# Optimization experiments

Hardware: AMD Instinct MI355X
Metric: run time of the kernel (lower is better)

Reference implementation:

```python
import jax, jax.numpy as jnp
import numpy as np

N = 100000
F_IN = 128
HIDDEN = 64
HEADS = 4
EPS = 1e-16
SLOPE = 0.2  # PyG GATConv default negative_slope


def gat_conv(x, src, dst, W, a_src, a_dst, b, heads, out_ch, concat, n_nodes):
    # x: [N, F]; W: [F, heads*out_ch]; a_src/a_dst: [heads, out_ch]
    h = (x @ W).reshape(n_nodes, heads, out_ch)              # [N, H, C]
    alpha_s = jnp.einsum('nhc,hc->nh', h, a_src)             # [N, H]
    alpha_d = jnp.einsum('nhc,hc->nh', h, a_dst)             # [N, H]
    e = alpha_s[src] + alpha_d[dst]                          # [E, H]
    e = jnp.where(e > 0, e, SLOPE * e)                       # leaky_relu
    # segment softmax over destination node
    m = jax.ops.segment_max(e, dst, num_segments=n_nodes)    # [N, H]
    m = jnp.where(jnp.isfinite(m), m, 0.0)                   # empty segments
    ex = jnp.exp(e - m[dst])                                 # [E, H]
    denom = jax.ops.segment_sum(ex, dst, num_segments=n_nodes)  # [N, H]
    alpha = ex / (denom[dst] + EPS)                          # [E, H]
    # weighted scatter-aggregate of source features at destinations
    msg = h[src] * alpha[:, :, None]                         # [E, H, C]
    out = jax.ops.segment_sum(msg, dst, num_segments=n_nodes)  # [N, H, C]
    if concat:
        out = out.reshape(n_nodes, heads * out_ch)
    else:
        out = out.mean(axis=1)
    return out + b


def setup_inputs() -> dict:
    key = jax.random.key(0)
    ks = jax.random.split(key, 12)
    x = jax.random.normal(ks[0], (N, F_IN), dtype=jnp.float32)
    edge_index = jax.random.randint(ks[1], (2, 1600000), 0, N, dtype=jnp.int64)
    s1 = 1.0 / np.sqrt(F_IN)
    s2 = 1.0 / np.sqrt(HIDDEN)
    return {
        'x': x,
        'edge_index': edge_index,
        'W1': jax.random.normal(ks[2], (F_IN, HIDDEN), dtype=jnp.float32) * s1,
        'a_src1': jax.random.normal(ks[3], (HEADS, HIDDEN // HEADS), dtype=jnp.float32) * s2,
        'a_dst1': jax.random.normal(ks[4], (HEADS, HIDDEN // HEADS), dtype=jnp.float32) * s2,
        'b1': jnp.zeros((HIDDEN,), dtype=jnp.float32),
        'W2': jax.random.normal(ks[5], (HIDDEN, HIDDEN), dtype=jnp.float32) * s2,
        'a_src2': jax.random.normal(ks[6], (1, HIDDEN), dtype=jnp.float32) * s2,
        'a_dst2': jax.random.normal(ks[7], (1, HIDDEN), dtype=jnp.float32) * s2,
        'b2': jnp.zeros((HIDDEN,), dtype=jnp.float32),
        'Wc': jax.random.normal(ks[8], (HIDDEN, 1), dtype=jnp.float32) * s2,
        'bc': jnp.zeros((1,), dtype=jnp.float32),
    }


def reference(x, edge_index, W1, a_src1, a_dst1, b1, W2, a_src2, a_dst2, b2, Wc, bc):
    src, dst = edge_index[0], edge_index[1]
    # dropout layers are identity in eval mode
    h = gat_conv(x, src, dst, W1, a_src1, a_dst1, b1,
                 heads=HEADS, out_ch=HIDDEN // HEADS, concat=True, n_nodes=N)
    h = jax.nn.relu(h)
    h = gat_conv(h, src, dst, W2, a_src2, a_dst2, b2,
                 heads=1, out_ch=HIDDEN, concat=False, n_nodes=N)
    h = jax.nn.relu(h)
    return h @ Wc + bc  # [N, 1]
```

## Files before the change

kernel.cpp:

```cpp
#include <hip/hip_runtime.h>
#include <hip/hip_bf16.h>


typedef __hip_bfloat16 bf16;
typedef unsigned short ushort;
typedef unsigned char uchar;
typedef __attribute__((ext_vector_type(8))) short short8;
typedef __attribute__((ext_vector_type(4))) float f32x4;

#define NN 100000
#define EE 1600000
#define BKB 9
#define BKN (1 << BKB)
#define NBK ((NN + BKN - 1) >> BKB)
#define CAP 10240
#define TILE 4096
#define EPT 16
#define NT ((EE + TILE - 1) / TILE)
#define BN 16
#define CHE 512

__device__ __forceinline__ float relu_np(float v) { return (v < 0.f) ? 0.f : v; }
__device__ __forceinline__ float lrelu(float v) { return v > 0.f ? v : 0.2f * v; }
__device__ __forceinline__ ushort f2bf(float f) {
    __hip_bfloat16 h = __float2bfloat16(f);
    return *reinterpret_cast<ushort*>(&h);
}
__device__ __forceinline__ float bf2f(ushort u) {
    unsigned int x = ((unsigned int)u) << 16;
    return __uint_as_float(x);
}

__global__ __launch_bounds__(256) void k_init(
    int* __restrict__ gcur, const float* __restrict__ W2,
    const float* __restrict__ aS2, const float* __restrict__ aD2,
    ushort* __restrict__ wExt)
{
    const int tid = threadIdx.x;
    if (tid < NBK) gcur[tid] = tid * CAP;
    for (int i = tid; i < 80 * 64; i += 256) {
        int n = i >> 6, k = i & 63;
        float v = 0.f;
        if (n < 64) {
            v = W2[k * 64 + n];
        } else if (n == 64) {
            for (int c = 0; c < 64; ++c) v = fmaf(W2[k * 64 + c], aS2[c], v);
        } else if (n == 65) {
            for (int c = 0; c < 64; ++c) v = fmaf(W2[k * 64 + c], aD2[c], v);
        }
        wExt[i] = f2bf(v);
    }
}

__global__ __launch_bounds__(256) void k_part(
    const int* __restrict__ src, const int* __restrict__ dst,
    int* __restrict__ gcur, int* __restrict__ pairs, int E)
{
    __shared__ int lh[NBK];
    __shared__ int lbase[NBK];
    const int tid = threadIdx.x;
    for (int i = tid; i < NBK; i += 256) lh[i] = 0;
    __syncthreads();
    const int e0 = blockIdx.x * TILE;
    int pk[EPT], bk[EPT], rv[EPT];
    #pragma unroll
    for (int j = 0; j < EPT; ++j) {
        int e = e0 + j * 256 + tid;
        if (e < E) {
            int d = dst[e];
            bk[j] = d >> BKB;
            pk[j] = src[e] | ((d & (BKN - 1)) << 17);
            rv[j] = atomicAdd(&lh[bk[j]], 1);
        }
    }
    __syncthreads();
    for (int i = tid; i < NBK; i += 256)
        lbase[i] = lh[i] ? atomicAdd(&gcur[i], lh[i]) : 0;
    __syncthreads();
    #pragma unroll
    for (int j = 0; j < EPT; ++j) {
        int e = e0 + j * 256 + tid;
        if (e < E) pairs[lbase[bk[j]] + rv[j]] = pk[j];
    }
}

__global__ __launch_bounds__(256) void k_bucket(
    const int* __restrict__ gcur, const int* __restrict__ pairs,
    int* __restrict__ row_ptr, uchar* __restrict__ rcnt,
    int* __restrict__ col, int N)
{
    __shared__ int hist[BKN];
    __shared__ int sP[256];
    const int b = blockIdx.x;
    const int n0 = b << BKB;
    const int tid = threadIdx.x;
    const int base = b * CAP, endE = gcur[b];
    for (int i = tid; i < BKN; i += 256) hist[i] = 0;
    __syncthreads();
    for (int i = base + tid; i < endE; i += 256)
        atomicAdd(&hist[pairs[i] >> 17], 1);
    __syncthreads();
    int a0 = hist[2 * tid], a1 = hist[2 * tid + 1];
    int tot = a0 + a1;
    sP[tid] = tot;
    __syncthreads();
    for (int off = 1; off < 256; off <<= 1) {
        int t = (tid >= off) ? sP[tid - off] : 0;
        __syncthreads();
        sP[tid] += t;
        __syncthreads();
    }
    const int excl = sP[tid] - tot;
    const int c0 = base + excl;
    hist[2 * tid] = c0;
    hist[2 * tid + 1] = c0 + a0;
    if (n0 + 2 * tid < N) {
        row_ptr[n0 + 2 * tid] = c0;
        rcnt[n0 + 2 * tid] = (uchar)a0;
    }
    if (n0 + 2 * tid + 1 < N) {
        row_ptr[n0 + 2 * tid + 1] = c0 + a0;
        rcnt[n0 + 2 * tid + 1] = (uchar)a1;
    }
    __syncthreads();
    for (int i = base + tid; i < endE; i += 256) {
        int pr = pairs[i];
        int p = atomicAdd(&hist[pr >> 17], 1);
        col[p] = pr & 0x1FFFF;
    }
}

__global__ __launch_bounds__(256) void k_gemm1(
    const float* __restrict__ x, const float* __restrict__ W1,
    const float* __restrict__ aS, const float* __restrict__ aD,
    ushort* __restrict__ h1, float* __restrict__ as1, float* __restrict__ ad1,
    int N)
{
    __shared__ ushort wB[64 * 128];
    __shared__ ushort wE[16 * 128];
    const int tid = threadIdx.x;
    for (int i = tid; i < 128 * 64; i += 256) {
        int k = i >> 6, n = i & 63;
        wB[n * 128 + k] = f2bf(W1[i]);
    }
    for (int i = tid; i < 128 * 16; i += 256) {
        int k = i >> 4, j = i & 15;
        float v = 0.f;
        if (j < 8) {
            int h = j & 3;
            const float* av = (j < 4) ? aS : aD;
            for (int c = 0; c < 16; ++c)
                v = fmaf(W1[k * 64 + h * 16 + c], av[h * 16 + c], v);
        }
        wE[j * 128 + k] = f2bf(v);
    }
    __syncthreads();
    const int w = tid >> 6, lane = tid & 63;
    const int m = lane & 15, quad = lane >> 4;
    const int ntiles = N >> 4;
    for (int tile = blockIdx.x * 4 + w; tile < ntiles; tile += gridDim.x * 4) {
        const int row0 = tile << 4;
        f32x4 acc[4] = {f32x4{0,0,0,0}, f32x4{0,0,0,0},
                        f32x4{0,0,0,0}, f32x4{0,0,0,0}};
        f32x4 acc5 = {0, 0, 0, 0};
        const float* xp = x + (size_t)(row0 + m) * 128 + quad * 8;
        #pragma unroll
        for (int ks = 0; ks < 128; ks += 32) {
            f32x4 x0 = *(const f32x4*)(xp + ks);
            f32x4 x1 = *(const f32x4*)(xp + ks + 4);
            short8 a;
            #pragma unroll
            for (int j = 0; j < 4; ++j) a[j] = (short)f2bf(x0[j]);
            #pragma unroll
            for (int j = 0; j < 4; ++j) a[4 + j] = (short)f2bf(x1[j]);
            #pragma unroll
            for (int t = 0; t < 4; ++t) {
                short8 b = *(const short8*)&wB[(t * 16 + m) * 128 + ks + quad * 8];
                acc[t] = __builtin_amdgcn_mfma_f32_16x16x32_bf16(a, b, acc[t], 0, 0, 0);
            }
            short8 b5 = *(const short8*)&wE[m * 128 + ks + quad * 8];
            acc5 = __builtin_amdgcn_mfma_f32_16x16x32_bf16(a, b5, acc5, 0, 0, 0);
        }
        #pragma unroll
        for (int t = 0; t < 4; ++t)
            #pragma unroll
            for (int r = 0; r < 4; ++r)
                h1[(size_t)(row0 + quad * 4 + r) * 64 + t * 16 + m] = f2bf(acc[t][r]);
        #pragma unroll
        for (int r = 0; r < 4; ++r) {
            int row = row0 + quad * 4 + r;
            if (m < 4) as1[row * 4 + m] = acc5[r];
            else if (m < 8) ad1[row * 4 + (m - 4)] = acc5[r];
        }
    }
}

__global__ __launch_bounds__(256, 8) void k_seg1f(
    const int* __restrict__ rp, const uchar* __restrict__ rcnt,
    const int* __restrict__ col,
    const float* __restrict__ as1, const float* __restrict__ ad1,
    const ushort* __restrict__ h1, const float* __restrict__ b1,
    const ushort* __restrict__ wExt,
    ushort* __restrict__ h2, float* __restrict__ as2, float* __restrict__ ad2,
    int N)
{
    __shared__ __align__(16) ushort zS[BN * 72];
    __shared__ float pS[CHE * 4];
    __shared__ int colS[CHE];
    __shared__ uchar ndS[CHE];
    __shared__ int sRp[BN + 1];
    __shared__ float bS[64];
    __shared__ float adS[BN * 4];

    const int tid = threadIdx.x;
    const int n0 = blockIdx.x * BN;

    if (tid < 64) bS[tid] = b1[tid];
    if (tid < BN * 4) adS[tid] = ad1[(size_t)n0 * 4 + tid];
    if (tid < BN) sRp[tid] = rp[n0 + tid];
    if (tid == BN) sRp[BN] = rp[n0 + BN - 1] + (int)rcnt[n0 + BN - 1];
    __syncthreads();

    const int eb0 = sRp[0];
    const int cnt = min(sRp[BN] - eb0, CHE);

    for (int t = tid; t < cnt; t += 256) {
        int ge = eb0 + t;
        colS[t] = col[ge];
        int nd = 0;
        #pragma unroll
        for (int k = 1; k < BN; ++k) nd += (ge >= sRp[k]);
        ndS[t] = (uchar)nd;
    }
    __syncthreads();
    for (int t = tid; t < cnt * 4; t += 256) {
        int e = t >> 2, hh = t & 3;
        float v = as1[(size_t)colS[e] * 4 + hh] + adS[ndS[e] * 4 + hh];
        pS[t] = __expf(lrelu(v));
    }
    __syncthreads();

    const int w = tid >> 6, lane = tid & 63;
    const int g = lane >> 4, c4 = lane & 15, head = c4 >> 2;
    const int nb = w * 4 + g;
    const int s_n = sRp[nb] - eb0, e_n = sRp[nb + 1] - eb0;

    f32x4 acc = {0, 0, 0, 0};
    float den = 0.f;
    int i = s_n;
    for (; i + 3 < e_n; i += 4) {
        int cA = colS[i], cB = colS[i + 1], cC = colS[i + 2], cD = colS[i + 3];
        ushort4 hA = *(const ushort4*)&h1[(size_t)cA * 64 + c4 * 4];
        ushort4 hB = *(const ushort4*)&h1[(size_t)cB * 64 + c4 * 4];
        ushort4 hC = *(const ushort4*)&h1[(size_t)cC * 64 + c4 * 4];
        ushort4 hD = *(const ushort4*)&h1[(size_t)cD * 64 + c4 * 4];
        float pA = pS[(i + 0) * 4 + head], pB = pS[(i + 1) * 4 + head];
        float pC = pS[(i + 2) * 4 + head], pD = pS[(i + 3) * 4 + head];
        den += (pA + pB) + (pC + pD);
        acc[0] = fmaf(pA, bf2f(hA.x), acc[0]);
        acc[1] = fmaf(pA, bf2f(hA.y), acc[1]);
        acc[2] = fmaf(pA, bf2f(hA.z), acc[2]);
        acc[3] = fmaf(pA, bf2f(hA.w), acc[3]);
        acc[0] = fmaf(pB, bf2f(hB.x), acc[0]);
        acc[1] = fmaf(pB, bf2f(hB.y), acc[1]);
        acc[2] = fmaf(pB, bf2f(hB.z), acc[2]);
        acc[3] = fmaf(pB, bf2f(hB.w), acc[3]);
        acc[0] = fmaf(pC, bf2f(hC.x), acc[0]);
        acc[1] = fmaf(pC, bf2f(hC.y), acc[1]);
        acc[2] = fmaf(pC, bf2f(hC.z), acc[2]);
        acc[3] = fmaf(pC, bf2f(hC.w), acc[3]);
        acc[0] = fmaf(pD, bf2f(hD.x), acc[0]);
        acc[1] = fmaf(pD, bf2f(hD.y), acc[1]);
        acc[2] = fmaf(pD, bf2f(hD.z), acc[2]);
        acc[3] = fmaf(pD, bf2f(hD.w), acc[3]);
    }
    for (; i < e_n; ++i) {
        int cA = colS[i];
        ushort4 hA = *(const ushort4*)&h1[(size_t)cA * 64 + c4 * 4];
        float pA = pS[i * 4 + head];
        den += pA;
        acc[0] = fmaf(pA, bf2f(hA.x), acc[0]);
        acc[1] = fmaf(pA, bf2f(hA.y), acc[1]);
        acc[2] = fmaf(pA, bf2f(hA.z), acc[2]);
        acc[3] = fmaf(pA, bf2f(hA.w), acc[3]);
    }
    {
        float inv = 1.f / (den + 1e-16f);
        ushort4 zv;
        zv.x = f2bf(relu_np(acc[0] * inv + bS[c4 * 4 + 0]));
        zv.y = f2bf(relu_np(acc[1] * inv + bS[c4 * 4 + 1]));
        zv.z = f2bf(relu_np(acc[2] * inv + bS[c4 * 4 + 2]));
        zv.w = f2bf(relu_np(acc[3] * inv + bS[c4 * 4 + 3]));
        *(ushort4*)&zS[nb * 72 + c4 * 4] = zv;
    }
    __syncthreads();

    const int m = c4, quad = g;
    for (int t = w; t < 5; t += 4) {
        f32x4 acct = {0, 0, 0, 0};
        #pragma unroll
        for (int ks = 0; ks < 64; ks += 32) {
            short8 a = *(const short8*)&zS[m * 72 + ks + quad * 8];
            short8 b = *(const short8*)&wExt[(t * 16 + m) * 64 + ks + quad * 8];
            acct = __builtin_amdgcn_mfma_f32_16x16x32_bf16(a, b, acct, 0, 0, 0);
        }
        if (t < 4) {
            #pragma unroll
            for (int r = 0; r < 4; ++r)
                h2[(size_t)(n0 + quad * 4 + r) * 64 + t * 16 + m] = f2bf(acct[r]);
        } else {
            #pragma unroll
            for (int r = 0; r < 4; ++r) {
                int row = n0 + quad * 4 + r;
                if (m == 0) as2[row] = acct[r];
                else if (m == 1) ad2[row] = acct[r];
            }
        }
    }
}

__global__ __launch_bounds__(256, 8) void k_seg2f(
    const int* __restrict__ rp, const uchar* __restrict__ rcnt,
    const int* __restrict__ col,
    const float* __restrict__ as2, const float* __restrict__ ad2,
    const ushort* __restrict__ h2, const float* __restrict__ b2,
    const float* __restrict__ Wc, const float* __restrict__ bc,
    float* __restrict__ out, int N)
{
    __shared__ float pS[CHE];
    __shared__ int colS[CHE];
    __shared__ uchar ndS[CHE];
    __shared__ int sRp[BN + 1];
    __shared__ float adS[BN];
    __shared__ float b2S[64];
    __shared__ float wcS[64];

    const int tid = threadIdx.x;
    const int n0 = blockIdx.x * BN;
    if (tid < 64) { b2S[tid] = b2[tid]; wcS[tid] = Wc[tid]; }
    if (tid < BN) { sRp[tid] = rp[n0 + tid]; adS[tid] = ad2[n0 + tid]; }
    if (tid == BN) sRp[BN] = rp[n0 + BN - 1] + (int)rcnt[n0 + BN - 1];
    __syncthreads();

    const int eb0 = sRp[0];
    const int cnt = min(sRp[BN] - eb0, CHE);
    for (int t = tid; t < cnt; t += 256) {
        int ge = eb0 + t;
        colS[t] = col[ge];
        int nd = 0;
        #pragma unroll
        for (int k = 1; k < BN; ++k) nd += (ge >= sRp[k]);
        ndS[t] = (uchar)nd;
    }
    __syncthreads();
    for (int t = tid; t < cnt; t += 256)
        pS[t] = __expf(lrelu(as2[colS[t]] + adS[ndS[t]]));
    __syncthreads();

    const int w = tid >> 6, lane = tid & 63;
    const int g = lane >> 4, c4 = lane & 15;
    const int nb = w * 4 + g;
    const int myn = n0 + nb;
    const int s_n = sRp[nb] - eb0, e_n = sRp[nb + 1] - eb0;

    f32x4 acc = {0, 0, 0, 0};
    float den = 0.f;
    int i = s_n;
    for (; i + 3 < e_n; i += 4) {
        int cA = colS[i], cB = colS[i + 1], cC = colS[i + 2], cD = colS[i + 3];
        ushort4 hA = *(const ushort4*)&h2[(size_t)cA * 64 + c4 * 4];
        ushort4 hB = *(const ushort4*)&h2[(size_t)cB * 64 + c4 * 4];
        ushort4 hC = *(const ushort4*)&h2[(size_t)cC * 64 + c4 * 4];
        ushort4 hD = *(const ushort4*)&h2[(size_t)cD * 64 + c4 * 4];
        float pA = pS[i + 0], pB = pS[i + 1], pC = pS[i + 2], pD = pS[i + 3];
        den += (pA + pB) + (pC + pD);
        acc[0] = fmaf(pA, bf2f(hA.x), acc[0]);
        acc[1] = fmaf(pA, bf2f(hA.y), acc[1]);
        acc[2] = fmaf(pA, bf2f(hA.z), acc[2]);
        acc[3] = fmaf(pA, bf2f(hA.w), acc[3]);
        acc[0] = fmaf(pB, bf2f(hB.x), acc[0]);
        acc[1] = fmaf(pB, bf2f(hB.y), acc[1]);
        acc[2] = fmaf(pB, bf2f(hB.z), acc[2]);
        acc[3] = fmaf(pB, bf2f(hB.w), acc[3]);
        acc[0] = fmaf(pC, bf2f(hC.x), acc[0]);
        acc[1] = fmaf(pC, bf2f(hC.y), acc[1]);
        acc[2] = fmaf(pC, bf2f(hC.z), acc[2]);
        acc[3] = fmaf(pC, bf2f(hC.w), acc[3]);
        acc[0] = fmaf(pD, bf2f(hD.x), acc[0]);
        acc[1] = fmaf(pD, bf2f(hD.y), acc[1]);
        acc[2] = fmaf(pD, bf2f(hD.z), acc[2]);
        acc[3] = fmaf(pD, bf2f(hD.w), acc[3]);
    }
    for (; i < e_n; ++i) {
        int cA = colS[i];
        ushort4 hA = *(const ushort4*)&h2[(size_t)cA * 64 + c4 * 4];
        float pA = pS[i];
        den += pA;
        acc[0] = fmaf(pA, bf2f(hA.x), acc[0]);
        acc[1] = fmaf(pA, bf2f(hA.y), acc[1]);
        acc[2] = fmaf(pA, bf2f(hA.z), acc[2]);
        acc[3] = fmaf(pA, bf2f(hA.w), acc[3]);
    }

    float inv = 1.f / (den + 1e-16f);
    float t2 = 0.f;
    #pragma unroll
    for (int j = 0; j < 4; ++j)
        t2 += relu_np(acc[j] * inv + b2S[c4 * 4 + j]) * wcS[c4 * 4 + j];
    t2 += __shfl_xor(t2, 1);
    t2 += __shfl_xor(t2, 2);
    t2 += __shfl_xor(t2, 4);
    t2 += __shfl_xor(t2, 8);
    if (c4 == 0) out[myn] = t2 + bc[0];
}

extern "C" void kernel_launch(void* const* d_in, const int* in_sizes, int n_in,
                              void* d_out, int out_size, void* d_ws, size_t ws_size,
                              hipStream_t stream)
{
    const float* x   = (const float*)d_in[0];
    const int*   ei  = (const int*)d_in[1];
    const float* W1  = (const float*)d_in[2];
    const float* aS1 = (const float*)d_in[3];
    const float* aD1 = (const float*)d_in[4];
    const float* b1  = (const float*)d_in[5];
    const float* W2  = (const float*)d_in[6];
    const float* aS2 = (const float*)d_in[7];
    const float* aD2 = (const float*)d_in[8];
    const float* b2  = (const float*)d_in[9];
    const float* Wc  = (const float*)d_in[10];
    const float* bc  = (const float*)d_in[11];
    float* out = (float*)d_out;

    const int N = NN;
    const int E = EE;
    const int* src = ei;
    const int* dst = ei + E;

    ushort* h1   = (ushort*)d_ws;
    ushort* h2   = h1 + (size_t)N * 64;
    float*  as1  = (float*)(h2 + (size_t)N * 64);
    float*  ad1  = as1 + (size_t)N * 4;
    float*  as2  = ad1 + (size_t)N * 4;
    float*  ad2  = as2 + (size_t)N;
    ushort* wExt = (ushort*)(ad2 + (size_t)N);
    int* row_ptr = (int*)(wExt + 80 * 64);
    uchar* rcnt  = (uchar*)(row_ptr + N);
    int* gcur    = (int*)(rcnt + ((N + 3) & ~3));
    int* col     = gcur + NBK;
    int* pairs   = (int*)h2;

    k_init<<<1, 256, 0, stream>>>(gcur, W2, aS2, aD2, wExt);
    k_part<<<NT, 256, 0, stream>>>(src, dst, gcur, pairs, E);
    k_bucket<<<NBK, 256, 0, stream>>>(gcur, pairs, row_ptr, rcnt, col, N);

    k_gemm1<<<782, 256, 0, stream>>>(x, W1, aS1, aD1, h1, as1, ad1, N);

    k_seg1f<<<N / BN, 256, 0, stream>>>(row_ptr, rcnt, col, as1, ad1, h1, b1,
                                        wExt, h2, as2, ad2, N);

    k_seg2f<<<N / BN, 256, 0, stream>>>(row_ptr, rcnt, col, as2, ad2, h2,
                                        b2, Wc, bc, out, N);
}
```

Measured before the change: 267.8 us.

## Fuse graph partitioning and bucketing with GEMM1 halves into shared launches

```diff
diff --git a/kernel.cpp b/kernel.cpp
--- a/kernel.cpp
+++ b/kernel.cpp
@@ -17,6 +17,8 @@
 #define TILE 4096
 #define EPT 16
 #define NT ((EE + TILE - 1) / TILE)
+#define GH 391
+#define GT 782
 #define BN 16
 #define CHE 512
 
@@ -31,113 +33,12 @@
     return __uint_as_float(x);
 }
 
-__global__ __launch_bounds__(256) void k_init(
-    int* __restrict__ gcur, const float* __restrict__ W2,
-    const float* __restrict__ aS2, const float* __restrict__ aD2,
-    ushort* __restrict__ wExt)
-{
-    const int tid = threadIdx.x;
-    if (tid < NBK) gcur[tid] = tid * CAP;
-    for (int i = tid; i < 80 * 64; i += 256) {
-        int n = i >> 6, k = i & 63;
-        float v = 0.f;
-        if (n < 64) {
-            v = W2[k * 64 + n];
-        } else if (n == 64) {
-            for (int c = 0; c < 64; ++c) v = fmaf(W2[k * 64 + c], aS2[c], v);
-        } else if (n == 65) {
-            for (int c = 0; c < 64; ++c) v = fmaf(W2[k * 64 + c], aD2[c], v);
-        }
-        wExt[i] = f2bf(v);
-    }
-}
-
-__global__ __launch_bounds__(256) void k_part(
-    const int* __restrict__ src, const int* __restrict__ dst,
-    int* __restrict__ gcur, int* __restrict__ pairs, int E)
-{
-    __shared__ int lh[NBK];
-    __shared__ int lbase[NBK];
-    const int tid = threadIdx.x;
-    for (int i = tid; i < NBK; i += 256) lh[i] = 0;
-    __syncthreads();
-    const int e0 = blockIdx.x * TILE;
-    int pk[EPT], bk[EPT], rv[EPT];
-    #pragma unroll
-    for (int j = 0; j < EPT; ++j) {
-        int e = e0 + j * 256 + tid;
-        if (e < E) {
-            int d = dst[e];
-            bk[j] = d >> BKB;
-            pk[j] = src[e] | ((d & (BKN - 1)) << 17);
-            rv[j] = atomicAdd(&lh[bk[j]], 1);
-        }
-    }
-    __syncthreads();
-    for (int i = tid; i < NBK; i += 256)
-        lbase[i] = lh[i] ? atomicAdd(&gcur[i], lh[i]) : 0;
-    __syncthreads();
-    #pragma unroll
-    for (int j = 0; j < EPT; ++j) {
-        int e = e0 + j * 256 + tid;
-        if (e < E) pairs[lbase[bk[j]] + rv[j]] = pk[j];
-    }
-}
-
-__global__ __launch_bounds__(256) void k_bucket(
-    const int* __restrict__ gcur, const int* __restrict__ pairs,
-    int* __restrict__ row_ptr, uchar* __restrict__ rcnt,
-    int* __restrict__ col, int N)
-{
-    __shared__ int hist[BKN];
-    __shared__ int sP[256];
-    const int b = blockIdx.x;
-    const int n0 = b << BKB;
-    const int tid = threadIdx.x;
-    const int base = b * CAP, endE = gcur[b];
-    for (int i = tid; i < BKN; i += 256) hist[i] = 0;
-    __syncthreads();
-    for (int i = base + tid; i < endE; i += 256)
-        atomicAdd(&hist[pairs[i] >> 17], 1);
-    __syncthreads();
-    int a0 = hist[2 * tid], a1 = hist[2 * tid + 1];
-    int tot = a0 + a1;
-    sP[tid] = tot;
-    __syncthreads();
-    for (int off = 1; off < 256; off <<= 1) {
-        int t = (tid >= off) ? sP[tid - off] : 0;
-        __syncthreads();
-        sP[tid] += t;
-        __syncthreads();
-    }
-    const int excl = sP[tid] - tot;
-    const int c0 = base + excl;
-    hist[2 * tid] = c0;
-    hist[2 * tid + 1] = c0 + a0;
-    if (n0 + 2 * tid < N) {
-        row_ptr[n0 + 2 * tid] = c0;
-        rcnt[n0 + 2 * tid] = (uchar)a0;
-    }
-    if (n0 + 2 * tid + 1 < N) {
-        row_ptr[n0 + 2 * tid + 1] = c0 + a0;
-        rcnt[n0 + 2 * tid + 1] = (uchar)a1;
-    }
-    __syncthreads();
-    for (int i = base + tid; i < endE; i += 256) {
-        int pr = pairs[i];
-        int p = atomicAdd(&hist[pr >> 17], 1);
-        col[p] = pr & 0x1FFFF;
-    }
-}
-
-__global__ __launch_bounds__(256) void k_gemm1(
+__device__ __forceinline__ void gemm1_body(
+    int gb, ushort* wB, ushort* wE,
     const float* __restrict__ x, const float* __restrict__ W1,
     const float* __restrict__ aS, const float* __restrict__ aD,
-    ushort* __restrict__ h1, float* __restrict__ as1, float* __restrict__ ad1,
-    int N)
-{
-    __shared__ ushort wB[64 * 128];
-    __shared__ ushort wE[16 * 128];
+    ushort* __restrict__ h1, float* __restrict__ as1, float* __restrict__ ad1)
+{
     const int tid = threadIdx.x;
     for (int i = tid; i < 128 * 64; i += 256) {
         int k = i >> 6, n = i & 63;
@@ -157,8 +58,8 @@
     __syncthreads();
     const int w = tid >> 6, lane = tid & 63;
     const int m = lane & 15, quad = lane >> 4;
-    const int ntiles = N >> 4;
-    for (int tile = blockIdx.x * 4 + w; tile < ntiles; tile += gridDim.x * 4) {
+    const int ntiles = NN >> 4;
+    for (int tile = gb * 4 + w; tile < ntiles; tile += GT * 4) {
         const int row0 = tile << 4;
         f32x4 acc[4] = {f32x4{0,0,0,0}, f32x4{0,0,0,0},
                         f32x4{0,0,0,0}, f32x4{0,0,0,0}};
@@ -192,6 +93,123 @@
             if (m < 4) as1[row * 4 + m] = acc5[r];
             else if (m < 8) ad1[row * 4 + (m - 4)] = acc5[r];
         }
+    }
+}
+
+__global__ __launch_bounds__(256) void k_pg(
+    const int* __restrict__ src, const int* __restrict__ dst,
+    int* __restrict__ gcur, int* __restrict__ pairs,
+    const float* __restrict__ x, const float* __restrict__ W1,
+    const float* __restrict__ aS, const float* __restrict__ aD,
+    ushort* __restrict__ h1, float* __restrict__ as1, float* __restrict__ ad1,
+    const float* __restrict__ W2, const float* __restrict__ aS2,
+    const float* __restrict__ aD2, ushort* __restrict__ wExt)
+{
+    __shared__ ushort wB[64 * 128];
+    __shared__ ushort wE[16 * 128];
+    __shared__ int lh[NBK];
+    __shared__ int lbase[NBK];
+    const int bid = blockIdx.x;
+    const int tid = threadIdx.x;
+
+    if (bid < NT) {
+        for (int i = tid; i < NBK; i += 256) lh[i] = 0;
+        __syncthreads();
+        const int e0 = bid * TILE;
+        int pk[EPT], bk[EPT], rv[EPT];
+        #pragma unroll
+        for (int j = 0; j < EPT; ++j) {
+            int e = e0 + j * 256 + tid;
+            if (e < EE) {
+                int d = dst[e];
+                bk[j] = d >> BKB;
+                pk[j] = src[e] | ((d & (BKN - 1)) << 17);
+                rv[j] = atomicAdd(&lh[bk[j]], 1);
+            }
+        }
+        __syncthreads();
+        for (int i = tid; i < NBK; i += 256)
+            lbase[i] = lh[i] ? atomicAdd(&gcur[i], lh[i]) : 0;
+        __syncthreads();
+        #pragma unroll
+        for (int j = 0; j < EPT; ++j) {
+            int e = e0 + j * 256 + tid;
+            if (e < EE)
+                pairs[(size_t)bk[j] * CAP + lbase[bk[j]] + rv[j]] = pk[j];
+        }
+    } else if (bid < NT + GH) {
+        gemm1_body(bid - NT, wB, wE, x, W1, aS, aD, h1, as1, ad1);
+    } else {
+        for (int i = tid; i < 80 * 64; i += 256) {
+            int n = i >> 6, k = i & 63;
+            float v = 0.f;
+            if (n < 64) {
+                v = W2[k * 64 + n];
+            } else if (n == 64) {
+                for (int c = 0; c < 64; ++c) v = fmaf(W2[k * 64 + c], aS2[c], v);
+            } else if (n == 65) {
+                for (int c = 0; c < 64; ++c) v = fmaf(W2[k * 64 + c], aD2[c], v);
+            }
+            wExt[i] = f2bf(v);
+        }
+    }
+}
+
+__global__ __launch_bounds__(256) void k_bg(
+    const int* __restrict__ gcur, const int* __restrict__ pairs,
+    int* __restrict__ row_ptr, uchar* __restrict__ rcnt,
+    int* __restrict__ col,
+    const float* __restrict__ x, const float* __restrict__ W1,
+    const float* __restrict__ aS, const float* __restrict__ aD,
+    ushort* __restrict__ h1, float* __restrict__ as1, float* __restrict__ ad1)
+{
+    __shared__ ushort wB[64 * 128];
+    __shared__ ushort wE[16 * 128];
+    __shared__ int hist[BKN];
+    __shared__ int sP[256];
+    const int bid = blockIdx.x;
+    const int tid = threadIdx.x;
+
+    if (bid >= NBK) {
+        gemm1_body(bid - NBK + GH, wB, wE, x, W1, aS, aD, h1, as1, ad1);
+        return;
+    }
+
+    const int b = bid;
+    const int n0 = b << BKB;
+    const int base = b * CAP, endE = base + gcur[b];
+    for (int i = tid; i < BKN; i += 256) hist[i] = 0;
+    __syncthreads();
+    for (int i = base + tid; i < endE; i += 256)
+        atomicAdd(&hist[pairs[i] >> 17], 1);
+    __syncthreads();
+    int a0 = hist[2 * tid], a1 = hist[2 * tid + 1];
+    int tot = a0 + a1;
+    sP[tid] = tot;
+    __syncthreads();
+    for (int off = 1; off < 256; off <<= 1) {
+        int t = (tid >= off) ? sP[tid - off] : 0;
+        __syncthreads();
+        sP[tid] += t;
+        __syncthreads();
+    }
+    const int excl = sP[tid] - tot;
+    const int c0 = base + excl;
+    hist[2 * tid] = c0;
+    hist[2 * tid + 1] = c0 + a0;
+    if (n0 + 2 * tid < NN) {
+        row_ptr[n0 + 2 * tid] = c0;
+        rcnt[n0 + 2 * tid] = (uchar)a0;
+    }
+    if (n0 + 2 * tid + 1 < NN) {
+        row_ptr[n0 + 2 * tid + 1] = c0 + a0;
+        rcnt[n0 + 2 * tid + 1] = (uchar)a1;
+    }
+    __syncthreads();
+    for (int i = base + tid; i < endE; i += 256) {
+        int pr = pairs[i];
+        int p = atomicAdd(&hist[pr >> 17], 1);
+        col[p] = pr & 0x1FFFF;
     }
 }
 
@@ -450,11 +468,14 @@
     int* col     = gcur + NBK;
     int* pairs   = (int*)h2;
 
-    k_init<<<1, 256, 0, stream>>>(gcur, W2, aS2, aD2, wExt);
-    k_part<<<NT, 256, 0, stream>>>(src, dst, gcur, pairs, E);
-    k_bucket<<<NBK, 256, 0, stream>>>(gcur, pairs, row_ptr, rcnt, col, N);
-
-    k_gemm1<<<782, 256, 0, stream>>>(x, W1, aS1, aD1, h1, as1, ad1, N);
+    hipMemsetAsync(gcur, 0, NBK * sizeof(int), stream);
+
+    k_pg<<<NT + GH + 1, 256, 0, stream>>>(src, dst, gcur, pairs,
+                                          x, W1, aS1, aD1, h1, as1, ad1,
+                                          W2, aS2, aD2, wExt);
+
+    k_bg<<<NBK + GH, 256, 0, stream>>>(gcur, pairs, row_ptr, rcnt, col,
+                                       x, W1, aS1, aD1, h1, as1, ad1);
 
     k_seg1f<<<N / BN, 256, 0, stream>>>(row_ptr, rcnt, col, as1, ad1, h1, b1,
                                         wExt, h2, as2, ad2, N);
```

New measurement: 252.6 us. -5.7%, faster.
